# Performance work log

Measured on AMD Instinct MI355X. Metric: run time of the kernel, lower is better.

The kernel has to match this reference:

```python
import jax, jax.numpy as jnp
import numpy as np

D_MODEL = 1024
N_HEADS = 16
HEAD_DIM = D_MODEL // N_HEADS
B, L = 2, 2048


def setup_inputs() -> dict:
    key = jax.random.key(0)
    ks = jax.random.split(key, 11)
    s = 1.0 / np.sqrt(D_MODEL)
    inp = {
        'query': jax.random.normal(ks[0], (B, L, D_MODEL), dtype=jnp.float32),
        'key': jax.random.normal(ks[1], (B, L, D_MODEL), dtype=jnp.float32),
        'value': jax.random.normal(ks[2], (B, L, D_MODEL), dtype=jnp.float32),
        'Wq_w': jax.random.normal(ks[3], (D_MODEL, D_MODEL), dtype=jnp.float32) * s,
        'Wq_b': jnp.zeros((D_MODEL,), dtype=jnp.float32),
        'Wk_w': jax.random.normal(ks[4], (D_MODEL, D_MODEL), dtype=jnp.float32) * s,
        'Wk_b': jnp.zeros((D_MODEL,), dtype=jnp.float32),
        'Wv_w': jax.random.normal(ks[5], (D_MODEL, D_MODEL), dtype=jnp.float32) * s,
        'Wv_b': jnp.zeros((D_MODEL,), dtype=jnp.float32),
        'Wo_w': jax.random.normal(ks[6], (D_MODEL, D_MODEL), dtype=jnp.float32) * s,
        'Wo_b': jnp.zeros((D_MODEL,), dtype=jnp.float32),
    }
    return inp


def reference(query, key, value, Wq_w, Wq_b, Wk_w, Wk_b, Wv_w, Wv_b, Wo_w, Wo_b):
    b = query.shape[0]
    # torch Linear: y = x @ W^T + b
    Q = query @ Wq_w.T + Wq_b
    K = key @ Wk_w.T + Wk_b
    V = value @ Wv_w.T + Wv_b
    # [B, L, D] -> [B, H, L, hd]
    def split_heads(x):
        return x.reshape(b, -1, N_HEADS, HEAD_DIM).transpose(0, 2, 1, 3)
    Qh, Kh, Vh = split_heads(Q), split_heads(K), split_heads(V)
    scale = 1.0 / jnp.sqrt(jnp.float32(HEAD_DIM))
    # energy: [B, H, Lq, Lk]
    energy = jnp.einsum('bhqd,bhkd->bhqk', Qh, Kh) * scale
    # NOTE: original code applies softmax over dim=1 (the HEADS axis) — faithful reproduction
    attn = jax.nn.softmax(energy, axis=1)
    out = jnp.einsum('bhqk,bhkd->bhqd', attn, Vh)  # [B, H, Lq, hd]
    out = out.transpose(0, 2, 1, 3).reshape(b, -1, D_MODEL)
    return out @ Wo_w.T + Wo_b
```

## Files before the change

### kernel.cpp

```cpp
#include <hip/hip_runtime.h>
#include <hip/hip_bf16.h>
#include <hip/hip_fp16.h>

#define DM 1024
#define NH 16
#define HD 64
#define LL 2048

typedef __attribute__((ext_vector_type(8))) short bf16x8;
typedef __attribute__((ext_vector_type(4))) float f32x4;

#define MFMA16(a,b,c) __builtin_amdgcn_mfma_f32_16x16x32_bf16((a),(b),(c),0,0,0)

#define GL16(g, l) __builtin_amdgcn_global_load_lds( \
    (const __attribute__((address_space(1))) unsigned int*)(g), \
    (__attribute__((address_space(3))) unsigned int*)(l), 16, 0, 0)

__device__ __forceinline__ ushort f2bf(float f) {
  union { float f; unsigned int u; } v; v.f = f;
  unsigned int u = v.u + 0x7fffu + ((v.u >> 16) & 1u);
  return (ushort)(u >> 16);
}

__global__ __launch_bounds__(256) void cvt6(const float* __restrict__ s0, ushort* __restrict__ d0, int n0,
                                            const float* __restrict__ s1, ushort* __restrict__ d1, int n1,
                                            const float* __restrict__ s2, ushort* __restrict__ d2, int n2,
                                            const float* __restrict__ s3, ushort* __restrict__ d3, int n3,
                                            const float* __restrict__ s4, ushort* __restrict__ d4, int n4,
                                            const float* __restrict__ s5, ushort* __restrict__ d5, int n5) {
  int i = (blockIdx.x * 256 + threadIdx.x) * 4;
  const float* s; ushort* d;
  if (i < n0) { s = s0; d = d0; }
  else if ((i -= n0) < n1) { s = s1; d = d1; }
  else if ((i -= n1) < n2) { s = s2; d = d2; }
  else if ((i -= n2) < n3) { s = s3; d = d3; }
  else if ((i -= n3) < n4) { s = s4; d = d4; }
  else if ((i -= n4) < n5) { s = s5; d = d5; }
  else return;
  float4 v = *(const float4*)(s + i);
  union { ushort u[4]; unsigned long long ll; } o;
  o.u[0] = f2bf(v.x); o.u[1] = f2bf(v.y); o.u[2] = f2bf(v.z); o.u[3] = f2bf(v.w);
  *(unsigned long long*)(d + i) = o.ll;
}

__global__ __launch_bounds__(256) void gemm_qkv(const ushort* __restrict__ qA, const ushort* __restrict__ qW,
                                                const float* __restrict__ qb, ushort* __restrict__ qO,
                                                const ushort* __restrict__ kA, const ushort* __restrict__ kW,
                                                const float* __restrict__ kb, ushort* __restrict__ kO,
                                                const ushort* __restrict__ vA, const ushort* __restrict__ vW,
                                                const float* __restrict__ vb, ushort* __restrict__ vO) {
  __shared__ ushort lA[2][64][64];
  __shared__ ushort lB[2][128][64];
  const int z = blockIdx.z;
  const ushort* Ab; const ushort* Wb; const float* bias; ushort* outp;
  float alpha; bool trans;
  if (z == 0)      { Ab = qA; Wb = qW; bias = qb; outp = qO; alpha = 0.125f; trans = false; }
  else if (z == 1) { Ab = kA; Wb = kW; bias = kb; outp = kO; alpha = 1.0f;   trans = false; }
  else             { Ab = vA; Wb = vW; bias = vb; outp = vO; alpha = 1.0f;   trans = true;  }

  const int m0 = blockIdx.x * 64, n0 = blockIdx.y * 128;
  const int t = threadIdx.x;
  const int w = t >> 6, lane = t & 63, lr = lane & 15, lg = lane >> 4;
  const int wm = (w >> 1) * 32, wn = (w & 1) * 64;
  const int lrow8 = lane >> 3;
  const int scol = ((lane & 7) ^ lrow8) * 8;

  f32x4 acc[2][4];
  #pragma unroll
  for (int i = 0; i < 2; ++i)
    #pragma unroll
    for (int j = 0; j < 4; ++j) acc[i][j] = (f32x4){0.f, 0.f, 0.f, 0.f};

  #pragma unroll
  for (int c = 0; c < 2; ++c)
    GL16(Ab + (m0 + w * 16 + c * 8 + lrow8) * DM + scol, &lA[0][w * 16 + c * 8][0]);
  #pragma unroll
  for (int c = 0; c < 4; ++c)
    GL16(Wb + (n0 + w * 32 + c * 8 + lrow8) * DM + scol, &lB[0][w * 32 + c * 8][0]);
  __syncthreads();

  int cur = 0;
  for (int k0 = 0; k0 < DM; k0 += 64) {
    if (k0 + 64 < DM) {
      #pragma unroll
      for (int c = 0; c < 2; ++c)
        GL16(Ab + (m0 + w * 16 + c * 8 + lrow8) * DM + k0 + 64 + scol, &lA[cur ^ 1][w * 16 + c * 8][0]);
      #pragma unroll
      for (int c = 0; c < 4; ++c)
        GL16(Wb + (n0 + w * 32 + c * 8 + lrow8) * DM + k0 + 64 + scol, &lB[cur ^ 1][w * 32 + c * 8][0]);
    }
    #pragma unroll
    for (int ks = 0; ks < 2; ++ks) {
      bf16x8 aF[2], bF[4];
      #pragma unroll
      for (int i = 0; i < 2; ++i)
        aF[i] = *(const bf16x8*)&lA[cur][wm + i * 16 + lr][(((ks * 4 + lg) ^ (lr & 7)) * 8)];
      #pragma unroll
      for (int j = 0; j < 4; ++j)
        bF[j] = *(const bf16x8*)&lB[cur][wn + j * 16 + lr][(((ks * 4 + lg) ^ (lr & 7)) * 8)];
      #pragma unroll
      for (int i = 0; i < 2; ++i)
        #pragma unroll
        for (int j = 0; j < 4; ++j)
          acc[i][j] = MFMA16(aF[i], bF[j], acc[i][j]);
    }
    __syncthreads();
    cur ^= 1;
  }

  #pragma unroll
  for (int i = 0; i < 2; ++i)
    #pragma unroll
    for (int j = 0; j < 4; ++j)
      #pragma unroll
      for (int r = 0; r < 4; ++r) {
        int m = m0 + wm + i * 16 + lg * 4 + r;
        int n = n0 + wn + j * 16 + lr;
        float v = (acc[i][j][r] + bias[n]) * alpha;
        int b = m >> 11, q = m & 2047, h = n >> 6, d = n & 63;
        if (!trans)
          outp[((b * NH + h) * LL + q) * HD + d] = f2bf(v);
        else
          outp[((b * NH + h) * HD + d) * LL + q] = f2bf(v);
      }
}

__global__ __launch_bounds__(256) void gemm_out(const ushort* __restrict__ Ab,
                                                const ushort* __restrict__ Wb,
                                                const float* __restrict__ bias,
                                                float* __restrict__ outf) {
  __shared__ ushort lA[2][64][64];
  __shared__ ushort lB[2][128][64];
  const int m0 = blockIdx.x * 64, n0 = blockIdx.y * 128;
  const int t = threadIdx.x;
  const int w = t >> 6, lane = t & 63, lr = lane & 15, lg = lane >> 4;
  const int wm = (w >> 1) * 32, wn = (w & 1) * 64;
  const int lrow8 = lane >> 3;
  const int scol = ((lane & 7) ^ lrow8) * 8;

  f32x4 acc[2][4];
  #pragma unroll
  for (int i = 0; i < 2; ++i)
    #pragma unroll
    for (int j = 0; j < 4; ++j) acc[i][j] = (f32x4){0.f, 0.f, 0.f, 0.f};

  #pragma unroll
  for (int c = 0; c < 2; ++c)
    GL16(Ab + (m0 + w * 16 + c * 8 + lrow8) * DM + scol, &lA[0][w * 16 + c * 8][0]);
  #pragma unroll
  for (int c = 0; c < 4; ++c)
    GL16(Wb + (n0 + w * 32 + c * 8 + lrow8) * DM + scol, &lB[0][w * 32 + c * 8][0]);
  __syncthreads();

  int cur = 0;
  for (int k0 = 0; k0 < DM; k0 += 64) {
    if (k0 + 64 < DM) {
      #pragma unroll
      for (int c = 0; c < 2; ++c)
        GL16(Ab + (m0 + w * 16 + c * 8 + lrow8) * DM + k0 + 64 + scol, &lA[cur ^ 1][w * 16 + c * 8][0]);
      #pragma unroll
      for (int c = 0; c < 4; ++c)
        GL16(Wb + (n0 + w * 32 + c * 8 + lrow8) * DM + k0 + 64 + scol, &lB[cur ^ 1][w * 32 + c * 8][0]);
    }
    #pragma unroll
    for (int ks = 0; ks < 2; ++ks) {
      bf16x8 aF[2], bF[4];
      #pragma unroll
      for (int i = 0; i < 2; ++i)
        aF[i] = *(const bf16x8*)&lA[cur][wm + i * 16 + lr][(((ks * 4 + lg) ^ (lr & 7)) * 8)];
      #pragma unroll
      for (int j = 0; j < 4; ++j)
        bF[j] = *(const bf16x8*)&lB[cur][wn + j * 16 + lr][(((ks * 4 + lg) ^ (lr & 7)) * 8)];
      #pragma unroll
      for (int i = 0; i < 2; ++i)
        #pragma unroll
        for (int j = 0; j < 4; ++j)
          acc[i][j] = MFMA16(aF[i], bF[j], acc[i][j]);
    }
    __syncthreads();
    cur ^= 1;
  }

  #pragma unroll
  for (int i = 0; i < 2; ++i)
    #pragma unroll
    for (int j = 0; j < 4; ++j)
      #pragma unroll
      for (int r = 0; r < 4; ++r) {
        int m = m0 + wm + i * 16 + lg * 4 + r;
        int n = n0 + wn + j * 16 + lr;
        outf[m * DM + n] = acc[i][j][r] + bias[n];
      }
}

__global__ __launch_bounds__(256) void pass_a_m(const ushort* __restrict__ Qh,
                                                const ushort* __restrict__ Kh,
                                                __half* __restrict__ rdenH) {
  __shared__ ushort lQ[128][72];
  __shared__ ushort lK[128][72];
  const int b = blockIdx.z, q0 = blockIdx.y * 128, k0 = blockIdx.x * 128;
  const int t = threadIdx.x, w = t >> 6, lane = t & 63, lr = lane & 15, lg = lane >> 4;

  f32x4 acc[2][8];
  #pragma unroll
  for (int i = 0; i < 2; ++i)
    #pragma unroll
    for (int j = 0; j < 8; ++j) acc[i][j] = (f32x4){0.f, 0.f, 0.f, 0.f};

  for (int h = 0; h < NH; ++h) {
    __syncthreads();
    #pragma unroll
    for (int u = 0; u < 4; ++u) {
      int c = u * 256 + t;
      int row = c >> 3, col = (c & 7) * 8;
      *(bf16x8*)&lQ[row][col] = *(const bf16x8*)&Qh[((b * NH + h) * LL + q0 + row) * HD + col];
      *(bf16x8*)&lK[row][col] = *(const bf16x8*)&Kh[((b * NH + h) * LL + k0 + row) * HD + col];
    }
    __syncthreads();
    #pragma unroll
    for (int i = 0; i < 2; ++i) {
      bf16x8 a0 = *(const bf16x8*)&lQ[w * 32 + i * 16 + lr][lg * 8];
      bf16x8 a1 = *(const bf16x8*)&lQ[w * 32 + i * 16 + lr][32 + lg * 8];
      #pragma unroll
      for (int j = 0; j < 8; ++j) {
        bf16x8 b0 = *(const bf16x8*)&lK[j * 16 + lr][lg * 8];
        bf16x8 b1 = *(const bf16x8*)&lK[j * 16 + lr][32 + lg * 8];
        f32x4 e = {0.f, 0.f, 0.f, 0.f};
        e = MFMA16(b0, a0, e);
        e = MFMA16(b1, a1, e);
        #pragma unroll
        for (int r = 0; r < 4; ++r) acc[i][j][r] += __expf(e[r]);
      }
    }
  }

  #pragma unroll
  for (int i = 0; i < 2; ++i)
    #pragma unroll
    for (int j = 0; j < 8; ++j) {
      int q = q0 + w * 32 + i * 16 + lr;
      int k = k0 + j * 16 + lg * 4;
      union { __half2 h2[2]; uint2 u; } pk;
      pk.h2[0] = __floats2half2_rn(__builtin_amdgcn_rcpf(acc[i][j][0]),
                                   __builtin_amdgcn_rcpf(acc[i][j][1]));
      pk.h2[1] = __floats2half2_rn(__builtin_amdgcn_rcpf(acc[i][j][2]),
                                   __builtin_amdgcn_rcpf(acc[i][j][3]));
      *(uint2*)&rdenH[(size_t)(b * LL + q) * LL + k] = pk.u;
    }
}

#define PB_BODY(PH)                                                              \
  {                                                                              \
    const int T = tt + PH;                                                       \
    const int k0 = T * 64;                                                       \
    uint2 rdN[4];                                                                \
    if (T + 1 < 32) {                                                            \
      GL16(Kh + (bh * LL + k0 + 64 + w * 8 + lrow8) * HD + scol,                 \
           &lK[PH ^ 1][w * 8][0]);                                               \
      GL16(Vt + (bh * HD + w * 8 + lrow8) * LL + k0 + 64 + scol,                 \
           &lV[PH ^ 1][w * 8][0]);                                               \
      _Pragma("unroll")                                                          \
      for (int j = 0; j < 4; ++j)                                                \
        rdN[j] = *(const uint2*)(rrow + k0 + 64 + j * 16 + lg * 4);              \
    }                                                                            \
    __builtin_amdgcn_s_setprio(1);                                               \
    if (T > 0) {                                                                 \
      bf16x8 aP0 = *(const bf16x8*)&U.p[PH ^ 1][w][lr][lg * 8];                  \
      bf16x8 aP1 = *(const bf16x8*)&U.p[PH ^ 1][w][lr][32 + lg * 8];             \
      _Pragma("unroll")                                                          \
      for (int j = 0; j < 4; ++j) {                                              \
        accO[j] = MFMA16(aP0, vF0[j], accO[j]);                                  \
        accO[j] = MFMA16(aP1, vF1[j], accO[j]);                                  \
      }                                                                          \
    }                                                                            \
    f32x4 e[4];                                                                  \
    _Pragma("unroll")                                                            \
    for (int j = 0; j < 4; ++j) {                                                \
      int krow = j * 16 + lr;                                                    \
      bf16x8 kf0 = *(const bf16x8*)&lK[PH][krow][((lg ^ (lr & 7)) * 8)];         \
      bf16x8 kf1 = *(const bf16x8*)&lK[PH][krow][(((4 + lg) ^ (lr & 7)) * 8)];   \
      e[j] = (f32x4){0.f, 0.f, 0.f, 0.f};                                        \
      e[j] = MFMA16(kf0, aQ0, e[j]);                                             \
      e[j] = MFMA16(kf1, aQ1, e[j]);                                             \
    }                                                                            \
    __builtin_amdgcn_s_setprio(0);                                               \
    _Pragma("unroll")                                                            \
    for (int j = 0; j < 4; ++j) {                                                \
      int vrow = j * 16 + lr;                                                    \
      vF0[j] = *(const bf16x8*)&lV[PH][vrow][((lg ^ (lr & 7)) * 8)];             \
      vF1[j] = *(const bf16x8*)&lV[PH][vrow][(((4 + lg) ^ (lr & 7)) * 8)];       \
    }                                                                            \
    _Pragma("unroll")                                                            \
    for (int j = 0; j < 4; ++j) {                                                \
      float2 f0 = __half22float2(*reinterpret_cast<const __half2*>(&rdC[j].x));  \
      float2 f1 = __half22float2(*reinterpret_cast<const __half2*>(&rdC[j].y));  \
      union { __hip_bfloat162 b2[2]; uint2 u; } pk;                              \
      pk.b2[0] = __float22bfloat162_rn(make_float2(__expf(e[j][0]) * f0.x,       \
                                                   __expf(e[j][1]) * f0.y));     \
      pk.b2[1] = __float22bfloat162_rn(make_float2(__expf(e[j][2]) * f1.x,       \
                                                   __expf(e[j][3]) * f1.y));     \
      *(uint2*)&U.p[PH][w][lr][j * 16 + lg * 4] = pk.u;                          \
    }                                                                            \
    if (T + 1 < 32) {                                                            \
      _Pragma("unroll")                                                          \
      for (int j = 0; j < 4; ++j) rdC[j] = rdN[j];                               \
    }                                                                            \
    __syncthreads();                                                             \
  }

__global__ __launch_bounds__(512, 4) void pass_b_m(const ushort* __restrict__ Qh,
                                                   const ushort* __restrict__ Kh,
                                                   const ushort* __restrict__ Vt,
                                                   const __half* __restrict__ rdenH,
                                                   ushort* __restrict__ AO) {
  __shared__ union UQP { ushort q[128][64]; ushort p[2][8][16][72]; } U;
  __shared__ ushort lK[2][64][64];
  __shared__ ushort lV[2][64][64];
  const int q0 = blockIdx.x * 128, h = blockIdx.y, b = blockIdx.z;
  const int t = threadIdx.x, w = t >> 6, lane = t & 63, lr = lane & 15, lg = lane >> 4;
  const int lrow8 = lane >> 3;
  const int scol = ((lane & 7) ^ lrow8) * 8;
  const int bh = b * NH + h;

  #pragma unroll
  for (int u = 0; u < 2; ++u) {
    int c = u * 512 + t;
    int row = c >> 3, col = (c & 7) * 8;
    *(bf16x8*)&U.q[row][col] = *(const bf16x8*)&Qh[(bh * LL + q0 + row) * HD + col];
  }
  GL16(Kh + (bh * LL + w * 8 + lrow8) * HD + scol, &lK[0][w * 8][0]);
  GL16(Vt + (bh * HD + w * 8 + lrow8) * LL + scol, &lV[0][w * 8][0]);
  const int qg = q0 + w * 16 + lr;
  const __half* rrow = rdenH + (size_t)(b * LL + qg) * LL;
  uint2 rdC[4];
  #pragma unroll
  for (int j = 0; j < 4; ++j) rdC[j] = *(const uint2*)(rrow + j * 16 + lg * 4);
  __syncthreads();

  bf16x8 aQ0 = *(const bf16x8*)&U.q[w * 16 + lr][lg * 8];
  bf16x8 aQ1 = *(const bf16x8*)&U.q[w * 16 + lr][32 + lg * 8];
  __syncthreads();

  f32x4 accO[4];
  #pragma unroll
  for (int j = 0; j < 4; ++j) accO[j] = (f32x4){0.f, 0.f, 0.f, 0.f};
  bf16x8 vF0[4], vF1[4];

  for (int tt = 0; tt < 32; tt += 2) {
    PB_BODY(0)
    PB_BODY(1)
  }

  {
    bf16x8 aP0 = *(const bf16x8*)&U.p[1][w][lr][lg * 8];
    bf16x8 aP1 = *(const bf16x8*)&U.p[1][w][lr][32 + lg * 8];
    #pragma unroll
    for (int j = 0; j < 4; ++j) {
      accO[j] = MFMA16(aP0, vF0[j], accO[j]);
      accO[j] = MFMA16(aP1, vF1[j], accO[j]);
    }
  }

  #pragma unroll
  for (int j = 0; j < 4; ++j)
    #pragma unroll
    for (int r = 0; r < 4; ++r) {
      int q = q0 + w * 16 + lg * 4 + r;
      int d = j * 16 + lr;
      AO[(b * LL + q) * DM + h * HD + d] = f2bf(accO[j][r]);
    }
}

extern "C" void kernel_launch(void* const* d_in, const int* in_sizes, int n_in,
                              void* d_out, int out_size, void* d_ws, size_t ws_size,
                              hipStream_t stream) {
  const float* query = (const float*)d_in[0];
  const float* key   = (const float*)d_in[1];
  const float* value = (const float*)d_in[2];
  const float* Wq_w  = (const float*)d_in[3];
  const float* Wq_b  = (const float*)d_in[4];
  const float* Wk_w  = (const float*)d_in[5];
  const float* Wk_b  = (const float*)d_in[6];
  const float* Wv_w  = (const float*)d_in[7];
  const float* Wv_b  = (const float*)d_in[8];
  const float* Wo_w  = (const float*)d_in[9];
  const float* Wo_b  = (const float*)d_in[10];

  char* ws = (char*)d_ws;
  char* dob = (char*)d_out;
  ushort* Qh  = (ushort*)(ws);
  ushort* Kh  = (ushort*)(ws + (8u  << 20));
  ushort* Vt  = (ushort*)(ws + (16u << 20));
  ushort* AO  = (ushort*)(ws + (24u << 20));
  ushort* qbf = (ushort*)(ws + (32u << 20));
  ushort* kbf = (ushort*)(ws + (40u << 20));
  ushort* Wob = (ushort*)(ws + (32u << 20));
  ushort* vbf = (ushort*)(dob);
  ushort* Wqb = (ushort*)(dob + (8u  << 20));
  ushort* Wkb = (ushort*)(dob + (10u << 20));
  ushort* Wvb = (ushort*)(dob + (12u << 20));
  __half* rdn = (__half*)d_out;

  const int NA = 2 * LL * DM;
  const int NW = DM * DM;

  cvt6<<<(3 * NA + 3 * NW) / 1024, 256, 0, stream>>>(
      query, qbf, NA, key, kbf, NA, value, vbf, NA,
      Wq_w, Wqb, NW, Wk_w, Wkb, NW, Wv_w, Wvb, NW);

  gemm_qkv<<<dim3(64, 8, 3), 256, 0, stream>>>(qbf, Wqb, Wq_b, Qh,
                                               kbf, Wkb, Wk_b, Kh,
                                               vbf, Wvb, Wv_b, Vt);

  cvt6<<<NW / 1024, 256, 0, stream>>>(Wo_w, Wob, NW,
                                      nullptr, nullptr, 0, nullptr, nullptr, 0,
                                      nullptr, nullptr, 0, nullptr, nullptr, 0,
                                      nullptr, nullptr, 0);

  pass_a_m<<<dim3(16, 16, 2), 256, 0, stream>>>(Qh, Kh, rdn);
  pass_b_m<<<dim3(16, NH, 2), 512, 0, stream>>>(Qh, Kh, Vt, rdn, AO);

  gemm_out<<<dim3(64, 8), 256, 0, stream>>>(AO, Wob, Wo_b, (float*)d_out);
}
```

Measured before the change: 223.4 us.

## Double-buffer async loads in pass_a, enlarge QKV GEMM tile, single P buffer

pass_a_m now double-buffers the per-head Q/K tiles. It uses asynchronous global-to-LDS loads with an XOR swizzle, so the next head is fetched while the current one is being computed. gemm_qkv grows its M tile from 64 to 128 rows, giving each wave 4x4 MFMA accumulators for more reuse, at the cost of fewer blocks and more registers. pass_b_m drops the double-buffered P staging area to a single per-wave buffer to cut LDS use, which relies on each wave reading its old P before writing the new one.

```diff
diff --git a/kernel.cpp b/kernel.cpp
--- a/kernel.cpp
+++ b/kernel.cpp
@@ -49,7 +49,7 @@
                                                 const float* __restrict__ kb, ushort* __restrict__ kO,
                                                 const ushort* __restrict__ vA, const ushort* __restrict__ vW,
                                                 const float* __restrict__ vb, ushort* __restrict__ vO) {
-  __shared__ ushort lA[2][64][64];
+  __shared__ ushort lA[2][128][64];
   __shared__ ushort lB[2][128][64];
   const int z = blockIdx.z;
   const ushort* Ab; const ushort* Wb; const float* bias; ushort* outp;
@@ -58,48 +58,46 @@
   else if (z == 1) { Ab = kA; Wb = kW; bias = kb; outp = kO; alpha = 1.0f;   trans = false; }
   else             { Ab = vA; Wb = vW; bias = vb; outp = vO; alpha = 1.0f;   trans = true;  }
 
-  const int m0 = blockIdx.x * 64, n0 = blockIdx.y * 128;
+  const int m0 = blockIdx.x * 128, n0 = blockIdx.y * 128;
   const int t = threadIdx.x;
   const int w = t >> 6, lane = t & 63, lr = lane & 15, lg = lane >> 4;
-  const int wm = (w >> 1) * 32, wn = (w & 1) * 64;
+  const int wm = (w >> 1) * 64, wn = (w & 1) * 64;
   const int lrow8 = lane >> 3;
   const int scol = ((lane & 7) ^ lrow8) * 8;
 
-  f32x4 acc[2][4];
-  #pragma unroll
-  for (int i = 0; i < 2; ++i)
+  f32x4 acc[4][4];
+  #pragma unroll
+  for (int i = 0; i < 4; ++i)
     #pragma unroll
     for (int j = 0; j < 4; ++j) acc[i][j] = (f32x4){0.f, 0.f, 0.f, 0.f};
 
   #pragma unroll
-  for (int c = 0; c < 2; ++c)
-    GL16(Ab + (m0 + w * 16 + c * 8 + lrow8) * DM + scol, &lA[0][w * 16 + c * 8][0]);
-  #pragma unroll
-  for (int c = 0; c < 4; ++c)
+  for (int c = 0; c < 4; ++c) {
+    GL16(Ab + (m0 + w * 32 + c * 8 + lrow8) * DM + scol, &lA[0][w * 32 + c * 8][0]);
     GL16(Wb + (n0 + w * 32 + c * 8 + lrow8) * DM + scol, &lB[0][w * 32 + c * 8][0]);
+  }
   __syncthreads();
 
   int cur = 0;
   for (int k0 = 0; k0 < DM; k0 += 64) {
     if (k0 + 64 < DM) {
       #pragma unroll
-      for (int c = 0; c < 2; ++c)
-        GL16(Ab + (m0 + w * 16 + c * 8 + lrow8) * DM + k0 + 64 + scol, &lA[cur ^ 1][w * 16 + c * 8][0]);
-      #pragma unroll
-      for (int c = 0; c < 4; ++c)
+      for (int c = 0; c < 4; ++c) {
+        GL16(Ab + (m0 + w * 32 + c * 8 + lrow8) * DM + k0 + 64 + scol, &lA[cur ^ 1][w * 32 + c * 8][0]);
         GL16(Wb + (n0 + w * 32 + c * 8 + lrow8) * DM + k0 + 64 + scol, &lB[cur ^ 1][w * 32 + c * 8][0]);
+      }
     }
     #pragma unroll
     for (int ks = 0; ks < 2; ++ks) {
-      bf16x8 aF[2], bF[4];
-      #pragma unroll
-      for (int i = 0; i < 2; ++i)
+      bf16x8 aF[4], bF[4];
+      #pragma unroll
+      for (int i = 0; i < 4; ++i)
         aF[i] = *(const bf16x8*)&lA[cur][wm + i * 16 + lr][(((ks * 4 + lg) ^ (lr & 7)) * 8)];
       #pragma unroll
       for (int j = 0; j < 4; ++j)
         bF[j] = *(const bf16x8*)&lB[cur][wn + j * 16 + lr][(((ks * 4 + lg) ^ (lr & 7)) * 8)];
       #pragma unroll
-      for (int i = 0; i < 2; ++i)
+      for (int i = 0; i < 4; ++i)
         #pragma unroll
         for (int j = 0; j < 4; ++j)
           acc[i][j] = MFMA16(aF[i], bF[j], acc[i][j]);
@@ -109,7 +107,7 @@
   }
 
   #pragma unroll
-  for (int i = 0; i < 2; ++i)
+  for (int i = 0; i < 4; ++i)
     #pragma unroll
     for (int j = 0; j < 4; ++j)
       #pragma unroll
@@ -196,10 +194,12 @@
 __global__ __launch_bounds__(256) void pass_a_m(const ushort* __restrict__ Qh,
                                                 const ushort* __restrict__ Kh,
                                                 __half* __restrict__ rdenH) {
-  __shared__ ushort lQ[128][72];
-  __shared__ ushort lK[128][72];
+  __shared__ ushort lQ[2][128][64];
+  __shared__ ushort lK[2][128][64];
   const int b = blockIdx.z, q0 = blockIdx.y * 128, k0 = blockIdx.x * 128;
   const int t = threadIdx.x, w = t >> 6, lane = t & 63, lr = lane & 15, lg = lane >> 4;
+  const int lrow8 = lane >> 3;
+  const int scol = ((lane & 7) ^ lrow8) * 8;
 
   f32x4 acc[2][8];
   #pragma unroll
@@ -207,24 +207,32 @@
     #pragma unroll
     for (int j = 0; j < 8; ++j) acc[i][j] = (f32x4){0.f, 0.f, 0.f, 0.f};
 
+  #pragma unroll
+  for (int c = 0; c < 4; ++c) {
+    GL16(Qh + ((b * NH) * LL + q0 + w * 32 + c * 8 + lrow8) * HD + scol, &lQ[0][w * 32 + c * 8][0]);
+    GL16(Kh + ((b * NH) * LL + k0 + w * 32 + c * 8 + lrow8) * HD + scol, &lK[0][w * 32 + c * 8][0]);
+  }
+  __syncthreads();
+
+  int cur = 0;
   for (int h = 0; h < NH; ++h) {
-    __syncthreads();
-    #pragma unroll
-    for (int u = 0; u < 4; ++u) {
-      int c = u * 256 + t;
-      int row = c >> 3, col = (c & 7) * 8;
-      *(bf16x8*)&lQ[row][col] = *(const bf16x8*)&Qh[((b * NH + h) * LL + q0 + row) * HD + col];
-      *(bf16x8*)&lK[row][col] = *(const bf16x8*)&Kh[((b * NH + h) * LL + k0 + row) * HD + col];
-    }
-    __syncthreads();
+    if (h + 1 < NH) {
+      #pragma unroll
+      for (int c = 0; c < 4; ++c) {
+        GL16(Qh + ((b * NH + h + 1) * LL + q0 + w * 32 + c * 8 + lrow8) * HD + scol, &lQ[cur ^ 1][w * 32 + c * 8][0]);
+        GL16(Kh + ((b * NH + h + 1) * LL + k0 + w * 32 + c * 8 + lrow8) * HD + scol, &lK[cur ^ 1][w * 32 + c * 8][0]);
+      }
+    }
     #pragma unroll
     for (int i = 0; i < 2; ++i) {
-      bf16x8 a0 = *(const bf16x8*)&lQ[w * 32 + i * 16 + lr][lg * 8];
-      bf16x8 a1 = *(const bf16x8*)&lQ[w * 32 + i * 16 + lr][32 + lg * 8];
+      int qrow = w * 32 + i * 16 + lr;
+      bf16x8 a0 = *(const bf16x8*)&lQ[cur][qrow][((lg ^ (lr & 7)) * 8)];
+      bf16x8 a1 = *(const bf16x8*)&lQ[cur][qrow][(((4 + lg) ^ (lr & 7)) * 8)];
       #pragma unroll
       for (int j = 0; j < 8; ++j) {
-        bf16x8 b0 = *(const bf16x8*)&lK[j * 16 + lr][lg * 8];
-        bf16x8 b1 = *(const bf16x8*)&lK[j * 16 + lr][32 + lg * 8];
+        int krow = j * 16 + lr;
+        bf16x8 b0 = *(const bf16x8*)&lK[cur][krow][((lg ^ (lr & 7)) * 8)];
+        bf16x8 b1 = *(const bf16x8*)&lK[cur][krow][(((4 + lg) ^ (lr & 7)) * 8)];
         f32x4 e = {0.f, 0.f, 0.f, 0.f};
         e = MFMA16(b0, a0, e);
         e = MFMA16(b1, a1, e);
@@ -232,6 +240,8 @@
         for (int r = 0; r < 4; ++r) acc[i][j][r] += __expf(e[r]);
       }
     }
+    __syncthreads();
+    cur ^= 1;
   }
 
   #pragma unroll
@@ -265,8 +275,8 @@
     }                                                                            \
     __builtin_amdgcn_s_setprio(1);                                               \
     if (T > 0) {                                                                 \
-      bf16x8 aP0 = *(const bf16x8*)&U.p[PH ^ 1][w][lr][lg * 8];                  \
-      bf16x8 aP1 = *(const bf16x8*)&U.p[PH ^ 1][w][lr][32 + lg * 8];             \
+      bf16x8 aP0 = *(const bf16x8*)&U.p[w][lr][lg * 8];                          \
+      bf16x8 aP1 = *(const bf16x8*)&U.p[w][lr][32 + lg * 8];                     \
       _Pragma("unroll")                                                          \
       for (int j = 0; j < 4; ++j) {                                              \
         accO[j] = MFMA16(aP0, vF0[j], accO[j]);                                  \
@@ -299,7 +309,7 @@
                                                    __expf(e[j][1]) * f0.y));     \
       pk.b2[1] = __float22bfloat162_rn(make_float2(__expf(e[j][2]) * f1.x,       \
                                                    __expf(e[j][3]) * f1.y));     \
-      *(uint2*)&U.p[PH][w][lr][j * 16 + lg * 4] = pk.u;                          \
+      *(uint2*)&U.p[w][lr][j * 16 + lg * 4] = pk.u;                              \
     }                                                                            \
     if (T + 1 < 32) {                                                            \
       _Pragma("unroll")                                                          \
@@ -313,7 +323,7 @@
                                                    const ushort* __restrict__ Vt,
                                                    const __half* __restrict__ rdenH,
                                                    ushort* __restrict__ AO) {
-  __shared__ union UQP { ushort q[128][64]; ushort p[2][8][16][72]; } U;
+  __shared__ union UQP { ushort q[128][64]; ushort p[8][16][72]; } U;
   __shared__ ushort lK[2][64][64];
   __shared__ ushort lV[2][64][64];
   const int q0 = blockIdx.x * 128, h = blockIdx.y, b = blockIdx.z;
@@ -352,8 +362,8 @@
   }
 
   {
-    bf16x8 aP0 = *(const bf16x8*)&U.p[1][w][lr][lg * 8];
-    bf16x8 aP1 = *(const bf16x8*)&U.p[1][w][lr][32 + lg * 8];
+    bf16x8 aP0 = *(const bf16x8*)&U.p[w][lr][lg * 8];
+    bf16x8 aP1 = *(const bf16x8*)&U.p[w][lr][32 + lg * 8];
     #pragma unroll
     for (int j = 0; j < 4; ++j) {
       accO[j] = MFMA16(aP0, vF0[j], accO[j]);
@@ -408,7 +418,7 @@
       query, qbf, NA, key, kbf, NA, value, vbf, NA,
       Wq_w, Wqb, NW, Wk_w, Wkb, NW, Wv_w, Wvb, NW);
 
-  gemm_qkv<<<dim3(64, 8, 3), 256, 0, stream>>>(qbf, Wqb, Wq_b, Qh,
+  gemm_qkv<<<dim3(32, 8, 3), 256, 0, stream>>>(qbf, Wqb, Wq_b, Qh,
                                                kbf, Wkb, Wk_b, Kh,
                                                vbf, Wvb, Wv_b, Vt);
 
```

Result: faster. 195.2 us (-12.6%).
